# Performance work log

Measured on AMD Instinct MI355X. Metric: run time of the kernel, lower is better.

The kernel has to match this reference:

```python
import jax, jax.numpy as jnp
import numpy as np

# Hard-coded dims from the module: 76 subcarriers * 12 data OFDM symbols = 912 data REs,
# QPSK (2 bits/sym), rate 1/2 -> n=1824, k=912; 4 tx streams, 8 rx antennas.
B, S, K = 512, 4, 912      # batch, streams, info bits (= data REs per stream)
R = 8                       # rx antennas
D = K                       # data resource elements per stream
N_CODE = 2 * K              # coded bits
SH1, SH2 = 7, 150           # circulant shifts of the LDPC-like code
BP_ITERS = 10
INV_SQRT2 = 0.7071067811865476

# check c connects info vars {c, c-7, c-150 (mod K)} and parity var K+c -> check degree 4
_c = np.arange(K)
VAR_IDX = jnp.asarray(np.stack([_c % K, (_c - SH1) % K, (_c - SH2) % K, K + _c], axis=1), jnp.int32)  # [K,4]


def setup_inputs() -> dict:
    key = jax.random.key(0)
    k1, k2, k3, k4, k5 = jax.random.split(key, 5)
    return {
        "b_bits": jax.random.randint(k1, (B, S, K), 0, 2, dtype=jnp.int32),
        "h_real": jax.random.normal(k2, (B, D, R, S), dtype=jnp.float32),
        "h_imag": jax.random.normal(k3, (B, D, R, S), dtype=jnp.float32),
        "n_real": jax.random.normal(k4, (B, D, R), dtype=jnp.float32),
        "n_imag": jax.random.normal(k5, (B, D, R), dtype=jnp.float32),
        "ebno_db": 10,
    }


def _bp_decode(llr):
    """Min-sum BP decode. llr: [B,S,N_CODE] demapper LLRs (log p1/p0). Returns hard info bits."""
    L = (-llr).reshape(B * S, N_CODE)          # internal convention log(p0/p1)
    vflat = VAR_IDX.reshape(-1)
    c2v = jnp.zeros((B * S, K, 4), L.dtype)
    pos = jnp.arange(4)
    for _ in range(BP_ITERS):
        ext = jnp.zeros_like(L).at[:, vflat].add(c2v.reshape(B * S, -1))
        tot = L + ext
        m_vc = tot[:, VAR_IDX] - c2v           # [BS,K,4] var->check
        a = jnp.abs(m_vc)
        srt = jnp.sort(a, -1)
        min1, min2 = srt[..., 0:1], srt[..., 1:2]
        amin = jnp.argmin(a, -1, keepdims=True)
        excl = jnp.where(pos == amin, min2, min1)   # leave-one-out min
        s = jnp.where(m_vc < 0, -1.0, 1.0)
        s_excl = jnp.prod(s, -1, keepdims=True) * s  # sign product excluding self
        c2v = s_excl * excl
    ext = jnp.zeros_like(L).at[:, vflat].add(c2v.reshape(B * S, -1))
    tot = L + ext
    return (tot[:, :K] < 0).astype(jnp.int32).reshape(B, S, K)


def reference(b_bits, h_real, h_imag, n_real, n_imag, ebno_db):
    no = 10.0 ** (-float(ebno_db) / 10.0)  # ebnodb2no with 2 bits/sym * rate 1/2
    # --- LDPC-like systematic circulant encode: p = A b mod 2, c = [b | p] ---
    p = (b_bits + jnp.roll(b_bits, SH1, -1) + jnp.roll(b_bits, SH2, -1)) % 2
    c = jnp.concatenate([b_bits, p], -1)                    # [B,S,N_CODE]
    # --- Gray QPSK mapper ---
    cb = c.reshape(B, S, K, 2).astype(jnp.float32)
    x = ((1.0 - 2.0 * cb[..., 0]) + 1j * (1.0 - 2.0 * cb[..., 1])) * INV_SQRT2  # [B,S,D]
    x_rg = jnp.transpose(x, (0, 2, 1))                      # [B,D,S]
    # --- normalized Rayleigh MIMO channel per RE + AWGN ---
    h = ((h_real + 1j * h_imag) * INV_SQRT2).astype(jnp.complex64)  # [B,D,R,S], E|h|^2=1
    noise = (n_real + 1j * n_imag).astype(jnp.complex64) * np.float32(np.sqrt(no * 0.5))
    y = jnp.einsum('bdrs,bds->bdr', h, x_rg) + noise        # [B,D,R]
    # --- per-RE LMMSE equalizer with Sionna-style bias normalization ---
    hH = jnp.conj(jnp.swapaxes(h, -1, -2))                  # [B,D,S,R]
    A = jnp.einsum('bdsr,bdrt->bdst', hH, h) + jnp.asarray(no, h.dtype) * jnp.eye(S, dtype=h.dtype)
    G = jnp.linalg.solve(A, hH)                             # [B,D,S,R]
    z = jnp.einsum('bdsr,bdr->bds', G, y)
    dgg = jnp.clip(jnp.real(jnp.einsum('bdsr,bdrs->bds', G, h)), 1e-6, 1.0 - 1e-6)
    x_hat = z / dgg.astype(jnp.complex64)
    no_eff = (1.0 - dgg) / dgg                              # [B,D,S]
    # --- exact APP QPSK demapper: llr = log p1/p0 ---
    scale = -2.0 * np.float32(np.sqrt(2.0)) / no_eff
    llr = jnp.stack([scale * jnp.real(x_hat), scale * jnp.imag(x_hat)], -1)  # [B,D,S,2]
    llr = jnp.transpose(llr, (0, 2, 1, 3)).reshape(B, S, N_CODE)
    # --- BP decode ---
    b_hat = _bp_decode(llr)
    return b_bits, b_hat
```

## Files before the change

kernel.cpp:

```cpp
#include <hip/hip_runtime.h>

#define B_ 512
#define S_ 4
#define K_ 912
#define R_ 8
#define D_ 912
#define NCODE 1824
#define BSK (B_*S_*K_)
#define BP_ITERS 10
#define NTH 228

__global__ void setup_kernel(const int* __restrict__ ebno, float* __restrict__ cst) {
  int ei = ebno[0];
  float ef = (ei >= -100 && ei <= 100) ? (float)ei : __int_as_float(ei);
  double no_d = pow(10.0, -(double)ef / 10.0);
  cst[0] = (float)no_d;
  cst[1] = (float)sqrt(no_d * 0.5);
}

#define BFLY1(v) { v += __shfl_xor(v, 1); }

__global__ __launch_bounds__(256) void mmse_llr_kernel(
    const int* __restrict__ bbits, const float* __restrict__ hre,
    const float* __restrict__ him, const float* __restrict__ nre,
    const float* __restrict__ nim, const float* __restrict__ cst,
    float* __restrict__ outf) {
#pragma clang fp contract(off)
  int t = blockIdx.x * 256 + threadIdx.x;
  int g = t >> 1;
  int half = t & 1;
  int b = g / D_;
  int d = g - b * D_;

  const float no_f = cst[0];
  const float nscale = cst[1];
  const float INV2 = 0.70710678118654752440f;

  float xr[S_], xq[S_];
  int k2 = 2 * d;
#pragma unroll
  for (int s = 0; s < S_; ++s) {
    const int* bb = bbits + (b * S_ + s) * K_;
    int c0, c1;
    if (k2 < K_) {
      c0 = bb[k2];
      c1 = bb[k2 + 1];
    } else {
      int j0 = k2 - K_, j1 = k2 + 1 - K_;
      int j0a = j0 - 7;   if (j0a < 0) j0a += K_;
      int j0b = j0 - 150; if (j0b < 0) j0b += K_;
      c0 = (bb[j0] + bb[j0a] + bb[j0b]) & 1;
      int j1a = j1 - 7;   if (j1a < 0) j1a += K_;
      int j1b = j1 - 150; if (j1b < 0) j1b += K_;
      c1 = (bb[j1] + bb[j1a] + bb[j1b]) & 1;
    }
    xr[s] = (1.0f - 2.0f * (float)c0) * INV2;
    xq[s] = (1.0f - 2.0f * (float)c1) * INV2;
  }

  float4 nr4v = reinterpret_cast<const float4*>(nre)[t];
  float4 ni4v = reinterpret_cast<const float4*>(nim)[t];
  float nrv[4] = {nr4v.x, nr4v.y, nr4v.z, nr4v.w};
  float niv[4] = {ni4v.x, ni4v.y, ni4v.z, ni4v.w};

  const float4* hre4 = reinterpret_cast<const float4*>(hre);
  const float4* him4 = reinterpret_cast<const float4*>(him);

  float Ad0=0.f, Ad1=0.f, Ad2=0.f, Ad3=0.f;
  float A10r=0.f,A10i=0.f,A20r=0.f,A20i=0.f,A21r=0.f,A21i=0.f;
  float A30r=0.f,A30i=0.f,A31r=0.f,A31i=0.f,A32r=0.f,A32i=0.f;
  float w0r=0.f,w0i=0.f,w1r=0.f,w1i=0.f,w2r=0.f,w2i=0.f,w3r=0.f,w3i=0.f;

#pragma unroll
  for (int q = 0; q < 4; ++q) {
    float4 h4r = hre4[(size_t)t * 4 + q];
    float4 h4i = him4[(size_t)t * 4 + q];
    float hr0=h4r.x*INV2, hr1=h4r.y*INV2, hr2=h4r.z*INV2, hr3=h4r.w*INV2;
    float hi0=h4i.x*INV2, hi1=h4i.y*INV2, hi2=h4i.z*INV2, hi3=h4i.w*INV2;
    float yr = 0.f, yi = 0.f;
    yr += hr0*xr[0] - hi0*xq[0]; yi += hr0*xq[0] + hi0*xr[0];
    yr += hr1*xr[1] - hi1*xq[1]; yi += hr1*xq[1] + hi1*xr[1];
    yr += hr2*xr[2] - hi2*xq[2]; yi += hr2*xq[2] + hi2*xr[2];
    yr += hr3*xr[3] - hi3*xq[3]; yi += hr3*xq[3] + hi3*xr[3];
    yr += nrv[q]*nscale; yi += niv[q]*nscale;
    Ad0 += hr0*hr0 + hi0*hi0;
    Ad1 += hr1*hr1 + hi1*hi1;
    Ad2 += hr2*hr2 + hi2*hi2;
    Ad3 += hr3*hr3 + hi3*hi3;
    A10r += hr1*hr0 + hi1*hi0;  A10i += hr1*hi0 - hi1*hr0;
    A20r += hr2*hr0 + hi2*hi0;  A20i += hr2*hi0 - hi2*hr0;
    A21r += hr2*hr1 + hi2*hi1;  A21i += hr2*hi1 - hi2*hr1;
    A30r += hr3*hr0 + hi3*hi0;  A30i += hr3*hi0 - hi3*hr0;
    A31r += hr3*hr1 + hi3*hi1;  A31i += hr3*hi1 - hi3*hr1;
    A32r += hr3*hr2 + hi3*hi2;  A32i += hr3*hi2 - hi3*hr2;
    w0r += hr0*yr + hi0*yi;  w0i += hr0*yi - hi0*yr;
    w1r += hr1*yr + hi1*yi;  w1i += hr1*yi - hi1*yr;
    w2r += hr2*yr + hi2*yi;  w2i += hr2*yi - hi2*yr;
    w3r += hr3*yr + hi3*yi;  w3i += hr3*yi - hi3*yr;
  }

  BFLY1(Ad0) BFLY1(Ad1) BFLY1(Ad2) BFLY1(Ad3)
  BFLY1(A10r) BFLY1(A10i) BFLY1(A20r) BFLY1(A20i) BFLY1(A21r) BFLY1(A21i)
  BFLY1(A30r) BFLY1(A30i) BFLY1(A31r) BFLY1(A31i) BFLY1(A32r) BFLY1(A32i)
  BFLY1(w0r) BFLY1(w0i) BFLY1(w1r) BFLY1(w1i)
  BFLY1(w2r) BFLY1(w2i) BFLY1(w3r) BFLY1(w3i)

  float Dv0 = Ad0 + no_f;
  float iD0 = 1.0f / Dv0;
  float L10r = A10r*iD0, L10i = A10i*iD0;
  float L20r = A20r*iD0, L20i = A20i*iD0;
  float L30r = A30r*iD0, L30i = A30i*iD0;
  float Dv1 = Ad1 + no_f - (L10r*L10r + L10i*L10i)*Dv0;
  float iD1 = 1.0f / Dv1;
  float t21r = A21r - (L20r*L10r + L20i*L10i)*Dv0;
  float t21i = A21i - (L20i*L10r - L20r*L10i)*Dv0;
  float L21r = t21r*iD1, L21i = t21i*iD1;
  float t31r = A31r - (L30r*L10r + L30i*L10i)*Dv0;
  float t31i = A31i - (L30i*L10r - L30r*L10i)*Dv0;
  float L31r = t31r*iD1, L31i = t31i*iD1;
  float Dv2 = Ad2 + no_f - (L20r*L20r + L20i*L20i)*Dv0 - (L21r*L21r + L21i*L21i)*Dv1;
  float iD2 = 1.0f / Dv2;
  float t32r = A32r - (L30r*L20r + L30i*L20i)*Dv0 - (L31r*L21r + L31i*L21i)*Dv1;
  float t32i = A32i - (L30i*L20r - L30r*L20i)*Dv0 - (L31i*L21r - L31r*L21i)*Dv1;
  float L32r = t32r*iD2, L32i = t32i*iD2;
  float Dv3 = Ad3 + no_f - (L30r*L30r + L30i*L30i)*Dv0 - (L31r*L31r + L31i*L31i)*Dv1
                        - (L32r*L32r + L32i*L32i)*Dv2;
  float iD3 = 1.0f / Dv3;

  float c0r = w0r, c0i = w0i;
  float c1r = w1r - (L10r*c0r - L10i*c0i);
  float c1i = w1i - (L10r*c0i + L10i*c0r);
  float c2r = w2r - (L20r*c0r - L20i*c0i) - (L21r*c1r - L21i*c1i);
  float c2i = w2i - (L20r*c0i + L20i*c0r) - (L21r*c1i + L21i*c1r);
  float c3r = w3r - (L30r*c0r - L30i*c0i) - (L31r*c1r - L31i*c1i) - (L32r*c2r - L32i*c2i);
  float c3i = w3i - (L30r*c0i + L30i*c0r) - (L31r*c1i + L31i*c1r) - (L32r*c2i + L32i*c2r);
  c0r *= iD0; c0i *= iD0;
  c1r *= iD1; c1i *= iD1;
  c2r *= iD2; c2i *= iD2;
  c3r *= iD3; c3i *= iD3;
  float z3r = c3r, z3i = c3i;
  float z2r = c2r - (L32r*z3r + L32i*z3i);
  float z2i = c2i - (L32r*z3i - L32i*z3r);
  float z1r = c1r - (L21r*z2r + L21i*z2i) - (L31r*z3r + L31i*z3i);
  float z1i = c1i - (L21r*z2i - L21i*z2r) - (L31r*z3i - L31i*z3r);
  float z0r = c0r - (L10r*z1r + L10i*z1i) - (L20r*z2r + L20i*z2i) - (L30r*z3r + L30i*z3i);
  float z0i = c0i - (L10r*z1i - L10i*z1r) - (L20r*z2i - L20i*z2r) - (L30r*z3i - L30i*z3r);

  float M10r = -L10r, M10i = -L10i;
  float M21r = -L21r, M21i = -L21i;
  float M32r = -L32r, M32i = -L32i;
  float M20r = -L20r - (L21r*M10r - L21i*M10i);
  float M20i = -L20i - (L21r*M10i + L21i*M10r);
  float M31r = -L31r - (L32r*M21r - L32i*M21i);
  float M31i = -L31i - (L32r*M21i + L32i*M21r);
  float M30r = -L30r - (L31r*M10r - L31i*M10i) - (L32r*M20r - L32i*M20i);
  float M30i = -L30i - (L31r*M10i + L31i*M10r) - (L32r*M20i + L32i*M20r);
  float Ai0 = iD0 + (M10r*M10r + M10i*M10i)*iD1 + (M20r*M20r + M20i*M20i)*iD2
                  + (M30r*M30r + M30i*M30i)*iD3;
  float Ai1 = iD1 + (M21r*M21r + M21i*M21i)*iD2 + (M31r*M31r + M31i*M31i)*iD3;
  float Ai2 = iD2 + (M32r*M32r + M32i*M32i)*iD3;
  float Ai3 = iD3;

  float zrv[4] = {z0r, z1r, z2r, z3r};
  float ziv[4] = {z0i, z1i, z2i, z3i};
  float Aiv[4] = {Ai0, Ai1, Ai2, Ai3};

#pragma unroll
  for (int j = 0; j < 2; ++j) {
    int s = half * 2 + j;
    float dgg = 1.0f - no_f * Aiv[s];
    float dg = fminf(fmaxf(dgg, 1e-6f), (float)(1.0 - 1e-6));
    float xhr = zrv[s] / dg;
    float xhi = ziv[s] / dg;
    float noe = (1.0f - dg) / dg;
    float sc = -2.8284270763397217f / noe;
    float2 o;
    o.x = -(sc * xhr);
    o.y = -(sc * xhi);
    size_t w = (size_t)(b * S_ + s);
    if (k2 < K_) {
      *reinterpret_cast<float2*>(outf + w * K_ + k2) = o;
    } else {
      *reinterpret_cast<float2*>(outf + (size_t)BSK + w * K_ + (k2 - K_)) = o;
    }
  }
}

__global__ __launch_bounds__(256) void bp_kernel(const int* __restrict__ bbits,
                                                 int* __restrict__ out) {
#pragma clang fp contract(off)
  __shared__ float tot[K_];
  __shared__ float E0[K_];
  __shared__ float E1[K_];
  __shared__ float E2[K_];
  int w = blockIdx.x;
  int tid = threadIdx.x;
  const float* outf = (const float*)out;
  bool act = tid < NTH;

  float Lv[4], LP[4];
  float c0v[4] = {0.f,0.f,0.f,0.f};
  float c1v[4] = {0.f,0.f,0.f,0.f};
  float c2v_[4] = {0.f,0.f,0.f,0.f};
  float c3v[4] = {0.f,0.f,0.f,0.f};

  if (act) {
#pragma unroll
    for (int k = 0; k < 4; ++k) {
      int n = tid + NTH * k;
      Lv[k] = outf[(size_t)w * K_ + n];
      LP[k] = outf[(size_t)BSK + (size_t)w * K_ + n];
      E0[n] = 0.f; E1[n] = 0.f; E2[n] = 0.f;
    }
  }
  __syncthreads();

  for (int it = 0; it < BP_ITERS; ++it) {
    if (act) {
#pragma unroll
      for (int k = 0; k < 4; ++k) {
        int n = tid + NTH * k;
        tot[n] = Lv[k] + ((E0[n] + E1[n]) + E2[n]);
      }
    }
    __syncthreads();
    if (act) {
#pragma unroll
      for (int k = 0; k < 4; ++k) {
        int c = tid + NTH * k;
        int i1 = c - 7;   if (i1 < 0) i1 += K_;
        int i2 = c - 150; if (i2 < 0) i2 += K_;
        float m0 = tot[c]  - c0v[k];
        float m1 = tot[i1] - c1v[k];
        float m2 = tot[i2] - c2v_[k];
        float totP = LP[k] + c3v[k];
        float m3 = totP - c3v[k];
        float a0 = fabsf(m0), a1 = fabsf(m1), a2 = fabsf(m2), a3 = fabsf(m3);
        float t01 = fminf(a0, a1), t23 = fminf(a2, a3);
        float e0 = fminf(a1, t23);
        float e1 = fminf(a0, t23);
        float e2 = fminf(t01, a3);
        float e3 = fminf(t01, a2);
        unsigned s0 = __float_as_uint(m0) & 0x80000000u;
        unsigned s1 = __float_as_uint(m1) & 0x80000000u;
        unsigned s2 = __float_as_uint(m2) & 0x80000000u;
        unsigned s3 = __float_as_uint(m3) & 0x80000000u;
        unsigned sp = (s0 ^ s1) ^ (s2 ^ s3);
        float n0 = __uint_as_float(__float_as_uint(e0) ^ (sp ^ s0));
        float n1 = __uint_as_float(__float_as_uint(e1) ^ (sp ^ s1));
        float n2 = __uint_as_float(__float_as_uint(e2) ^ (sp ^ s2));
        float n3 = __uint_as_float(__float_as_uint(e3) ^ (sp ^ s3));
        c0v[k] = n0; c1v[k] = n1; c2v_[k] = n2; c3v[k] = n3;
        E0[c] = n0; E1[i1] = n1; E2[i2] = n2;
      }
    }
    __syncthreads();
  }

  if (act) {
#pragma unroll
    for (int k = 0; k < 4; ++k) {
      int n = tid + NTH * k;
      float ttt = Lv[k] + ((E0[n] + E1[n]) + E2[n]);
      out[(size_t)BSK + (size_t)w * K_ + n] = (ttt < 0.f) ? 1 : 0;
      out[(size_t)w * K_ + n] = bbits[(size_t)w * K_ + n];
    }
  }
}

extern "C" void kernel_launch(void* const* d_in, const int* in_sizes, int n_in,
                              void* d_out, int out_size, void* d_ws, size_t ws_size,
                              hipStream_t stream) {
  const int*   b_bits = (const int*)d_in[0];
  const float* h_real = (const float*)d_in[1];
  const float* h_imag = (const float*)d_in[2];
  const float* n_real = (const float*)d_in[3];
  const float* n_imag = (const float*)d_in[4];
  const int*   ebno   = (const int*)d_in[5];
  int* out = (int*)d_out;
  float* cst = (float*)d_ws;

  setup_kernel<<<1, 1, 0, stream>>>(ebno, cst);
  mmse_llr_kernel<<<(B_ * D_ * 2) / 256, 256, 0, stream>>>(
      b_bits, h_real, h_imag, n_real, n_imag, cst, (float*)d_out);
  bp_kernel<<<B_ * S_, 256, 0, stream>>>(b_bits, out);
}
```

Baseline: 61.17 us.

## Precompute packed QPSK code bytes in a separate kernel and hoist channel loads

Adds a pre-pass kernel that encodes the parity bits and packs each resource element's 8 coded bits into one byte in workspace. The MMSE/LLR kernel then reads one byte instead of doing redundant scattered int loads, and builds symbol values with sign-bit XOR. In the original, both threads of a pair repeated those loads. The channel and noise loads are also issued up front, before symbol construction, so memory latency can overlap. The cost is an extra kernel launch and a byte-array round trip through memory; a fallback path handles a workspace that is too small.

```diff
diff --git a/kernel.cpp b/kernel.cpp
--- a/kernel.cpp
+++ b/kernel.cpp
@@ -9,6 +9,7 @@
 #define BSK (B_*S_*K_)
 #define BP_ITERS 10
 #define NTH 228
+#define CODES_OFF 16
 
 __global__ void setup_kernel(const int* __restrict__ ebno, float* __restrict__ cst) {
   int ei = ebno[0];
@@ -18,53 +19,103 @@
   cst[1] = (float)sqrt(no_d * 0.5);
 }
 
+__global__ __launch_bounds__(256) void pack_codes_kernel(
+    const int* __restrict__ bbits, unsigned char* __restrict__ codes) {
+  int g = blockIdx.x * 256 + threadIdx.x;
+  int b = g / D_;
+  int d = g - b * D_;
+  int k2 = 2 * d;
+  unsigned code = 0;
+#pragma unroll
+  for (int s = 0; s < S_; ++s) {
+    const int* bb = bbits + (b * S_ + s) * K_;
+    unsigned c0, c1;
+    if (k2 < K_) {
+      c0 = (unsigned)bb[k2];
+      c1 = (unsigned)bb[k2 + 1];
+    } else {
+      int j0 = k2 - K_, j1 = k2 + 1 - K_;
+      int j0a = j0 - 7;   if (j0a < 0) j0a += K_;
+      int j0b = j0 - 150; if (j0b < 0) j0b += K_;
+      c0 = (unsigned)(bb[j0] + bb[j0a] + bb[j0b]) & 1u;
+      int j1a = j1 - 7;   if (j1a < 0) j1a += K_;
+      int j1b = j1 - 150; if (j1b < 0) j1b += K_;
+      c1 = (unsigned)(bb[j1] + bb[j1a] + bb[j1b]) & 1u;
+    }
+    code |= (c0 << (2 * s)) | (c1 << (2 * s + 1));
+  }
+  codes[g] = (unsigned char)code;
+}
+
 #define BFLY1(v) { v += __shfl_xor(v, 1); }
 
+template <bool USE_CODES>
 __global__ __launch_bounds__(256) void mmse_llr_kernel(
     const int* __restrict__ bbits, const float* __restrict__ hre,
     const float* __restrict__ him, const float* __restrict__ nre,
     const float* __restrict__ nim, const float* __restrict__ cst,
-    float* __restrict__ outf) {
+    const unsigned char* __restrict__ codes, float* __restrict__ outf) {
 #pragma clang fp contract(off)
   int t = blockIdx.x * 256 + threadIdx.x;
   int g = t >> 1;
   int half = t & 1;
   int b = g / D_;
   int d = g - b * D_;
+  int k2 = 2 * d;
 
   const float no_f = cst[0];
   const float nscale = cst[1];
   const float INV2 = 0.70710678118654752440f;
 
-  float xr[S_], xq[S_];
-  int k2 = 2 * d;
-#pragma unroll
-  for (int s = 0; s < S_; ++s) {
-    const int* bb = bbits + (b * S_ + s) * K_;
-    int c0, c1;
-    if (k2 < K_) {
-      c0 = bb[k2];
-      c1 = bb[k2 + 1];
-    } else {
-      int j0 = k2 - K_, j1 = k2 + 1 - K_;
-      int j0a = j0 - 7;   if (j0a < 0) j0a += K_;
-      int j0b = j0 - 150; if (j0b < 0) j0b += K_;
-      c0 = (bb[j0] + bb[j0a] + bb[j0b]) & 1;
-      int j1a = j1 - 7;   if (j1a < 0) j1a += K_;
-      int j1b = j1 - 150; if (j1b < 0) j1b += K_;
-      c1 = (bb[j1] + bb[j1a] + bb[j1b]) & 1;
-    }
-    xr[s] = (1.0f - 2.0f * (float)c0) * INV2;
-    xq[s] = (1.0f - 2.0f * (float)c1) * INV2;
-  }
-
+  const float4* hre4 = reinterpret_cast<const float4*>(hre);
+  const float4* him4 = reinterpret_cast<const float4*>(him);
+  float4 hR0 = hre4[(size_t)t * 4 + 0];
+  float4 hR1 = hre4[(size_t)t * 4 + 1];
+  float4 hR2 = hre4[(size_t)t * 4 + 2];
+  float4 hR3 = hre4[(size_t)t * 4 + 3];
+  float4 hI0 = him4[(size_t)t * 4 + 0];
+  float4 hI1 = him4[(size_t)t * 4 + 1];
+  float4 hI2 = him4[(size_t)t * 4 + 2];
+  float4 hI3 = him4[(size_t)t * 4 + 3];
   float4 nr4v = reinterpret_cast<const float4*>(nre)[t];
   float4 ni4v = reinterpret_cast<const float4*>(nim)[t];
+
+  float xr[S_], xq[S_];
+  if (USE_CODES) {
+    unsigned code = codes[g];
+#pragma unroll
+    for (int s = 0; s < S_; ++s) {
+      unsigned c0 = (code >> (2 * s)) & 1u;
+      unsigned c1 = (code >> (2 * s + 1)) & 1u;
+      xr[s] = __uint_as_float(0x3F3504F3u ^ (c0 << 31));
+      xq[s] = __uint_as_float(0x3F3504F3u ^ (c1 << 31));
+    }
+  } else {
+#pragma unroll
+    for (int s = 0; s < S_; ++s) {
+      const int* bb = bbits + (b * S_ + s) * K_;
+      int c0, c1;
+      if (k2 < K_) {
+        c0 = bb[k2];
+        c1 = bb[k2 + 1];
+      } else {
+        int j0 = k2 - K_, j1 = k2 + 1 - K_;
+        int j0a = j0 - 7;   if (j0a < 0) j0a += K_;
+        int j0b = j0 - 150; if (j0b < 0) j0b += K_;
+        c0 = (bb[j0] + bb[j0a] + bb[j0b]) & 1;
+        int j1a = j1 - 7;   if (j1a < 0) j1a += K_;
+        int j1b = j1 - 150; if (j1b < 0) j1b += K_;
+        c1 = (bb[j1] + bb[j1a] + bb[j1b]) & 1;
+      }
+      xr[s] = (1.0f - 2.0f * (float)c0) * INV2;
+      xq[s] = (1.0f - 2.0f * (float)c1) * INV2;
+    }
+  }
+
   float nrv[4] = {nr4v.x, nr4v.y, nr4v.z, nr4v.w};
   float niv[4] = {ni4v.x, ni4v.y, ni4v.z, ni4v.w};
-
-  const float4* hre4 = reinterpret_cast<const float4*>(hre);
-  const float4* him4 = reinterpret_cast<const float4*>(him);
+  float4 hRq[4] = {hR0, hR1, hR2, hR3};
+  float4 hIq[4] = {hI0, hI1, hI2, hI3};
 
   float Ad0=0.f, Ad1=0.f, Ad2=0.f, Ad3=0.f;
   float A10r=0.f,A10i=0.f,A20r=0.f,A20i=0.f,A21r=0.f,A21i=0.f;
@@ -73,8 +124,8 @@
 
 #pragma unroll
   for (int q = 0; q < 4; ++q) {
-    float4 h4r = hre4[(size_t)t * 4 + q];
-    float4 h4i = him4[(size_t)t * 4 + q];
+    float4 h4r = hRq[q];
+    float4 h4i = hIq[q];
     float hr0=h4r.x*INV2, hr1=h4r.y*INV2, hr2=h4r.z*INV2, hr3=h4r.w*INV2;
     float hi0=h4i.x*INV2, hi1=h4i.y*INV2, hi2=h4i.z*INV2, hi3=h4i.w*INV2;
     float yr = 0.f, yi = 0.f;
@@ -279,9 +330,17 @@
   const int*   ebno   = (const int*)d_in[5];
   int* out = (int*)d_out;
   float* cst = (float*)d_ws;
+  unsigned char* codes = (unsigned char*)d_ws + CODES_OFF;
+  bool use_codes = ws_size >= (size_t)(CODES_OFF + B_ * D_);
 
   setup_kernel<<<1, 1, 0, stream>>>(ebno, cst);
-  mmse_llr_kernel<<<(B_ * D_ * 2) / 256, 256, 0, stream>>>(
-      b_bits, h_real, h_imag, n_real, n_imag, cst, (float*)d_out);
+  if (use_codes) {
+    pack_codes_kernel<<<(B_ * D_) / 256, 256, 0, stream>>>(b_bits, codes);
+    mmse_llr_kernel<true><<<(B_ * D_ * 2) / 256, 256, 0, stream>>>(
+        b_bits, h_real, h_imag, n_real, n_imag, cst, codes, (float*)d_out);
+  } else {
+    mmse_llr_kernel<false><<<(B_ * D_ * 2) / 256, 256, 0, stream>>>(
+        b_bits, h_real, h_imag, n_real, n_imag, cst, codes, (float*)d_out);
+  }
   bp_kernel<<<B_ * S_, 256, 0, stream>>>(b_bits, out);
 }
```

New measurement: 65.90 us. 7.7% more time.
